# Kernel optimization log

Measured on AMD Instinct MI355X. Metric: run time of the kernel, lower is better.

## Reference

```python
import jax, jax.numpy as jnp
import numpy as np

B, D0, D1 = 4096, 128, 128
T, DEPTH, W = 64, 2, 4          # num_tree, depth, width
S = W ** (DEPTH + 1)            # num_state = 64
NODES = sum(W ** l for l in range(DEPTH + 1))  # 21 internal nodes per tree
D = D0 + D1


def setup_inputs() -> dict:
    key = jax.random.key(0)
    ks = jax.random.split(key, 9)
    inp0 = jax.random.normal(ks[0], (B, D0), jnp.float32)
    inp1 = jax.random.normal(ks[1], (B, D1), jnp.float32)
    x2 = jax.random.normal(ks[2], (B,), jnp.float32)
    # ForestLinear: per-tree, per-node linear maps to `width` branch logits
    W_nodes = 0.02 * jax.random.normal(ks[3], (T, NODES, D, W), jnp.float32)
    b_nodes = jnp.zeros((T, NODES, W), jnp.float32)
    # MultiDense([0,1], 1): per-(tree,state) linear probe per input
    W0 = 0.02 * jax.random.normal(ks[4], (T, S, D0), jnp.float32)
    b0 = jnp.zeros((T, S), jnp.float32)
    W1 = 0.02 * jax.random.normal(ks[5], (T, S, D1), jnp.float32)
    b1 = jnp.zeros((T, S), jnp.float32)
    return {"inp0": inp0, "inp1": inp1, "x2": x2,
            "W_nodes": W_nodes, "b_nodes": b_nodes,
            "W0": W0, "b0": b0, "W1": W1, "b1": b1}


def _forest_states(x, W_nodes, b_nodes):
    # x: [B, D] -> leaf-state probabilities [B, T, S]
    logits = jnp.einsum('bd,tndw->btnw', x, W_nodes) + b_nodes  # [B,T,NODES,W]
    probs = jax.nn.softmax(logits, axis=-1)
    p = jnp.ones((x.shape[0], T, 1), probs.dtype)
    off = 0
    for l in range(DEPTH + 1):
        n = W ** l
        pl = probs[:, :, off:off + n, :]                 # [B,T,n,W]
        p = (p[..., None] * pl).reshape(x.shape[0], T, n * W)
        off += n
    return p  # [B, T, S]


def reference(inp0, inp1, x2, W_nodes, b_nodes, W0, b0, W1, b1):
    x_states = _forest_states(jnp.concatenate([inp0, inp1], axis=-1), W_nodes, b_nodes)
    # per-tree/state linear probes; equivalent to tile + MultiDense, no materialized tile
    x_pred = (jnp.einsum('bd,tsd->bts', inp0, W0) + b0
              + jnp.einsum('bd,tsd->bts', inp1, W1) + b1)  # [B,T,S]
    y_pred_logit_parallel = x2[:, None, None] + x_pred
    ave_pred_tree = jnp.sum(x_states * jax.nn.sigmoid(y_pred_logit_parallel), axis=2)  # [B,T]
    ave_pred = jnp.mean(ave_pred_tree, axis=1)  # [B]
    return (y_pred_logit_parallel, ave_pred)
```

## Files before the change

### kernel.cpp

```cpp
#include <hip/hip_runtime.h>

#define B_SZ    4096
#define DD      256
#define T_TREES 64
#define NNODES  21
#define S_LEAF  64
#define M_TILE  256
#define HBYTES  40960
#define WBYTES  (2 * HBYTES)
#define XOFF    ((size_t)T_TREES * WBYTES)
#define QBYTES  20480


typedef __attribute__((ext_vector_type(8))) short  short8;
typedef __attribute__((ext_vector_type(4))) float  f32x4;

#define DPP_ADD(x, ctrl) ((x) + __int_as_float(__builtin_amdgcn_mov_dpp(__float_as_int(x), (ctrl), 0xF, 0xF, true)))
#define DPP_MOV(x, ctrl) __int_as_float(__builtin_amdgcn_mov_dpp(__float_as_int(x), (ctrl), 0xF, 0xF, true))
__device__ __forceinline__ float qsum4(float x) {
    x = DPP_ADD(x, 0xB1);
    x = DPP_ADD(x, 0x4E);
    return x;
}
__device__ __forceinline__ float rsum16(float x) {
    x = DPP_ADD(x, 0xB1);
    x = DPP_ADD(x, 0x4E);
    x = DPP_ADD(x, 0x124);
    x = DPP_ADD(x, 0x128);
    return x;
}

__device__ __forceinline__ unsigned short f2bf(float f) {
    unsigned int u = __float_as_uint(f);
    u += 0x7fffu + ((u >> 16) & 1u);
    return (unsigned short)(u >> 16);
}
__device__ __forceinline__ void gl2lds16(const void* g, void* l) {
    __builtin_amdgcn_global_load_lds(
        (const __attribute__((address_space(1))) unsigned int*)g,
        (__attribute__((address_space(3))) unsigned int*)l, 16, 0, 0);
}
__device__ __host__ __forceinline__ int woffh(int c, int klo) {
    return c * 256 + (((klo ^ c) & 15) << 4);
}
__device__ __host__ __forceinline__ int woffq(int c, int klo) {
    return (c >> 1) * 256 + (((((klo << 1) ^ (c & 14))) | (c & 1)) << 4);
}

__global__ void zero_ave_kernel(float* __restrict__ out1) {
    int i = blockIdx.x * 256 + threadIdx.x;
    if (i < B_SZ) out1[i] = 0.0f;
}

__global__ void prep_weights(const float* __restrict__ Wn, const float* __restrict__ W0,
                             const float* __restrict__ W1, const float* __restrict__ inp0,
                             const float* __restrict__ inp1, char* __restrict__ ws,
                             float* __restrict__ out1) {
    int id = blockIdx.x * 256 + threadIdx.x;
    if (id < 43008) {
        int oct  = id & 31;
        int rest = id >> 5;
        int n    = rest % NNODES;
        int t    = rest / NNODES;
        int h    = oct >> 4, klo = oct & 15;
        const f32x4* src = (const f32x4*)(Wn + (((size_t)t * NNODES + n) * DD + oct * 8) * 4);
        f32x4 v[8];
        #pragma unroll
        for (int j = 0; j < 8; ++j) v[j] = src[j];
        char* base = ws + (size_t)t * WBYTES + h * HBYTES;
        #pragma unroll
        for (int w = 0; w < 4; ++w) {
            int c = n * 4 + w + (n >= 5 ? 12 : 0);
            short8 pack;
            #pragma unroll
            for (int j = 0; j < 8; ++j) pack[j] = (short)f2bf(v[j][w]);
            *(short8*)(base + woffh(c, klo)) = pack;
        }
    } else if (id < 67584) {
        int idx  = id - 43008;
        int kc   = idx & 31;
        int rest = idx >> 5;
        int c    = 20 + rest % 12;
        int t    = rest / 12;
        short8 z = (short8){0,0,0,0,0,0,0,0};
        *(short8*)(ws + (size_t)t * WBYTES + (kc >> 4) * HBYTES + woffh(c, kc & 15)) = z;
    } else if (id < 198656) {
        int idx = id - 67584;
        int kc  = idx & 31;
        int s   = (idx >> 5) & 63;
        int t   = idx >> 11;
        int k0  = kc * 8;
        const float* src = (k0 < 128) ? (W0 + ((size_t)t * S_LEAF + s) * 128 + k0)
                                      : (W1 + ((size_t)t * S_LEAF + s) * 128 + (k0 - 128));
        short8 pack;
        #pragma unroll
        for (int j = 0; j < 8; ++j) pack[j] = (short)f2bf(src[j]);
        *(short8*)(ws + (size_t)t * WBYTES + (kc >> 4) * HBYTES + woffh(96 + s, kc & 15)) = pack;
    } else if (id < 202752) {
        out1[id - 198656] = 0.0f;
    } else if (id < 333824) {
        int idx = id - 202752;
        int oct = idx & 31;
        int r   = idx >> 5;
        const float* src = (oct < 16) ? (inp0 + (size_t)r * 128 + oct * 8)
                                      : (inp1 + (size_t)r * 128 + (oct - 16) * 8);
        f32x4 f0 = *(const f32x4*)src;
        f32x4 f1 = *(const f32x4*)(src + 4);
        short8 pack;
        pack[0]=(short)f2bf(f0[0]); pack[1]=(short)f2bf(f0[1]);
        pack[2]=(short)f2bf(f0[2]); pack[3]=(short)f2bf(f0[3]);
        pack[4]=(short)f2bf(f1[0]); pack[5]=(short)f2bf(f1[1]);
        pack[6]=(short)f2bf(f1[2]); pack[7]=(short)f2bf(f1[3]);
        *(short8*)(ws + XOFF + ((size_t)r * DD + oct * 8) * 2) = pack;
    }
}

__global__ __launch_bounds__(512, 4)
void forest_main(const float* __restrict__ x2,  const float* __restrict__ bn,
                 const float* __restrict__ b0,  const float* __restrict__ b1,
                 const char* __restrict__ wsW,
                 float* __restrict__ out0, float* __restrict__ out1) {
    __shared__ __align__(16) char smem[HBYTES];

    const int tid  = threadIdx.x;
    const int orig = blockIdx.x;
    const int swz  = (orig & 7) * 128 + (orig >> 3);
    const int t    = swz >> 4;
    const int mt   = swz & 15;
    const int m0   = mt * M_TILE;
    const int lane = tid & 63;
    const int wid  = tid >> 6;
    const int ri   = lane & 15;
    const int kg   = lane >> 4;

    const unsigned short* xbf = (const unsigned short*)(wsW + XOFF);
    const char* wbase = wsW + (size_t)t * WBYTES;

    f32x4 acc[2][10];
    #pragma unroll
    for (int sr = 0; sr < 2; ++sr)
        #pragma unroll
        for (int ct = 0; ct < 10; ++ct)
            acc[sr][ct] = (f32x4){0.f, 0.f, 0.f, 0.f};

    const int gr0r = m0 + wid * 32 + ri;
    const int gr1r = gr0r + 16;
    const unsigned short* aBase0 = xbf + (size_t)gr0r * DD + kg * 8;
    const unsigned short* aBase1 = xbf + (size_t)gr1r * DD + kg * 8;

    for (int h = 0; h < 2; ++h) {
        {
            const char* src = wbase + h * HBYTES + tid * 16;
            char* dst = smem + tid * 16;
            #pragma unroll
            for (int it = 0; it < 5; ++it)
                gl2lds16(src + it * 8192, dst + it * 8192);
        }
        short8 a0 = *(const short8*)(aBase0 + (h * 4) * 32);
        short8 a1 = *(const short8*)(aBase1 + (h * 4) * 32);
        __syncthreads();

        #pragma unroll
        for (int ks = 0; ks < 4; ++ks) {
            short8 n0, n1;
            if (ks < 3) {
                n0 = *(const short8*)(aBase0 + (h * 4 + ks + 1) * 32);
                n1 = *(const short8*)(aBase1 + (h * 4 + ks + 1) * 32);
            }
            const int klo = ks * 4 + kg;
            const int dsB = ri * 256 + (((klo ^ ri) & 15) << 4);
            #pragma unroll
            for (int ct = 0; ct < 10; ++ct) {
                short8 bv = *(const short8*)(smem + dsB + ct * 4096);
                acc[0][ct] = __builtin_amdgcn_mfma_f32_16x16x32_bf16(a0, bv, acc[0][ct], 0, 0, 0);
                acc[1][ct] = __builtin_amdgcn_mfma_f32_16x16x32_bf16(a1, bv, acc[1][ct], 0, 0, 0);
            }
            a0 = n0; a1 = n1;
        }
        if (h == 0) __syncthreads();
    }

    const int kgbase = kg * 16;
    #pragma unroll
    for (int sr = 0; sr < 2; ++sr) {
        const int rlBase = wid * 32 + sr * 16 + kg * 4;
        const int gr0 = m0 + rlBase;
        f32x4 x2v = *(const f32x4*)(x2 + gr0);
        float bn0 = bn[t * 84 + ri];
        float bn1 = bn[t * 84 + 16 + (ri & 3)];

        float L1r[4];
        #pragma unroll
        for (int r = 0; r < 4; ++r) {
            float e0 = __expf(acc[sr][0][r] + bn0);
            float p0 = e0 * __builtin_amdgcn_rcpf(qsum4(e0));
            float e1 = __expf(acc[sr][1][r] + bn1);
            float p1 = e1 * __builtin_amdgcn_rcpf(qsum4(e1));
            float pa  = __shfl(p0, kgbase + (ri >> 2));
            float pb0 = DPP_MOV(p0, 0x124);
            float pb1 = DPP_MOV(p1, 0x124);
            L1r[r] = pa * ((ri < 12) ? pb0 : pb1);
        }
        float partial[4] = {0.f, 0.f, 0.f, 0.f};
        #pragma unroll
        for (int ct = 0; ct < 4; ++ct) {
            int s = ct * 16 + ri;
            float bn2 = bn[t * 84 + 20 + s];
            float bb  = b0[t * S_LEAF + s] + b1[t * S_LEAF + s];
            #pragma unroll
            for (int r = 0; r < 4; ++r) {
                float e = __expf(acc[sr][2 + ct][r] + bn2);
                float p2 = e * __builtin_amdgcn_rcpf(qsum4(e));
                float L2 = p2 * __shfl(L1r[r], kgbase + ct * 4 + (ri >> 2));
                float y = acc[sr][6 + ct][r] + x2v[r] + bb;
                out0[((size_t)(gr0 + r) * T_TREES + t) * S_LEAF + s] = y;
                float sg = __builtin_amdgcn_rcpf(1.0f + __expf(-y));
                partial[r] += sg * L2;
            }
        }
        #pragma unroll
        for (int r = 0; r < 4; ++r) {
            float p = rsum16(partial[r]);
            if (ri == 0) atomicAdd(out1 + gr0 + r, p * (1.0f / T_TREES));
        }
    }
}

__device__ __forceinline__ short8 ldAraw(const float* __restrict__ inp0,
                                         const float* __restrict__ inp1,
                                         int gr, int kkidx, int kg) {
    int k0 = kkidx * 32 + kg * 8;
    const float* src = (k0 < 128) ? (inp0 + (size_t)gr * 128 + k0)
                                  : (inp1 + (size_t)gr * 128 + (k0 - 128));
    f32x4 f0 = *(const f32x4*)src;
    f32x4 f1 = *(const f32x4*)(src + 4);
    short8 a;
    a[0]=(short)f2bf(f0[0]); a[1]=(short)f2bf(f0[1]);
    a[2]=(short)f2bf(f0[2]); a[3]=(short)f2bf(f0[3]);
    a[4]=(short)f2bf(f1[0]); a[5]=(short)f2bf(f1[1]);
    a[6]=(short)f2bf(f1[2]); a[7]=(short)f2bf(f1[3]);
    return a;
}

__global__ __launch_bounds__(256, 2)
void forest_fb(const float* __restrict__ inp0, const float* __restrict__ inp1,
               const float* __restrict__ x2,   const float* __restrict__ Wn,
               const float* __restrict__ bn,   const float* __restrict__ W0,
               const float* __restrict__ b0,   const float* __restrict__ W1,
               const float* __restrict__ b1,
               float* __restrict__ out0, float* __restrict__ out1) {
    __shared__ __align__(16) char smem[QBYTES];

    const int tid  = threadIdx.x;
    const int orig = blockIdx.x;
    const int swz  = (orig & 7) * 256 + (orig >> 3);
    const int t    = swz >> 5;
    const int mt   = swz & 31;
    const int m0   = mt * 128;
    const int lane = tid & 63;
    const int wid  = tid >> 6;
    const int ri   = lane & 15;
    const int kg   = lane >> 4;

    f32x4 acc[2][10];
    #pragma unroll
    for (int sr = 0; sr < 2; ++sr)
        #pragma unroll
        for (int ct = 0; ct < 10; ++ct)
            acc[sr][ct] = (f32x4){0.f, 0.f, 0.f, 0.f};

    const int gr0r = m0 + wid * 32 + ri;
    const int gr1r = gr0r + 16;

    int dsb[2];
    #pragma unroll
    for (int kkl = 0; kkl < 2; ++kkl) {
        int klo = kkl * 4 + kg;
        dsb[kkl] = (ri >> 1) * 256 + (((((klo << 1) ^ (ri & 14))) | (ri & 1)) << 4);
    }

    for (int q = 0; q < 4; ++q) {
        #pragma unroll
        for (int it = 0; it < 5; ++it) {
            int idx = tid + it * 256;
            int c   = idx >> 3;
            int klo = idx & 7;
            int k0  = (q * 8 + klo) * 8;
            unsigned short v[8];
            if (c < 20) {
                int n = c >> 2, w = c & 3;
                const float* src = Wn + (((size_t)t * NNODES + n) * DD + k0) * 4 + w;
                #pragma unroll
                for (int j = 0; j < 8; ++j) v[j] = f2bf(src[j * 4]);
            } else if (c < 32) {
                #pragma unroll
                for (int j = 0; j < 8; ++j) v[j] = 0;
            } else if (c < 96) {
                int n = 5 + ((c - 32) >> 2), w = (c - 32) & 3;
                const float* src = Wn + (((size_t)t * NNODES + n) * DD + k0) * 4 + w;
                #pragma unroll
                for (int j = 0; j < 8; ++j) v[j] = f2bf(src[j * 4]);
            } else {
                int s = c - 96;
                const float* src = (k0 < 128) ? (W0 + ((size_t)t * S_LEAF + s) * 128 + k0)
                                              : (W1 + ((size_t)t * S_LEAF + s) * 128 + (k0 - 128));
                #pragma unroll
                for (int j = 0; j < 8; ++j) v[j] = f2bf(src[j]);
            }
            short8 pack;
            #pragma unroll
            for (int j = 0; j < 8; ++j) pack[j] = (short)v[j];
            *(short8*)(smem + woffq(c, klo)) = pack;
        }
        short8 a00 = ldAraw(inp0, inp1, gr0r, 2*q+0, kg);
        short8 a10 = ldAraw(inp0, inp1, gr1r, 2*q+0, kg);
        short8 a01 = ldAraw(inp0, inp1, gr0r, 2*q+1, kg);
        short8 a11 = ldAraw(inp0, inp1, gr1r, 2*q+1, kg);
        __syncthreads();
        #pragma unroll
        for (int ct = 0; ct < 10; ++ct) {
            short8 b0f = *(const short8*)(smem + dsb[0] + ct * 2048);
            acc[0][ct] = __builtin_amdgcn_mfma_f32_16x16x32_bf16(a00, b0f, acc[0][ct], 0, 0, 0);
            acc[1][ct] = __builtin_amdgcn_mfma_f32_16x16x32_bf16(a10, b0f, acc[1][ct], 0, 0, 0);
        }
        #pragma unroll
        for (int ct = 0; ct < 10; ++ct) {
            short8 b1f = *(const short8*)(smem + dsb[1] + ct * 2048);
            acc[0][ct] = __builtin_amdgcn_mfma_f32_16x16x32_bf16(a01, b1f, acc[0][ct], 0, 0, 0);
            acc[1][ct] = __builtin_amdgcn_mfma_f32_16x16x32_bf16(a11, b1f, acc[1][ct], 0, 0, 0);
        }
        if (q < 3) __syncthreads();
    }

    const int kgbase = kg * 16;
    #pragma unroll
    for (int sr = 0; sr < 2; ++sr) {
        const int rlBase = wid * 32 + sr * 16 + kg * 4;
        const int gr0 = m0 + rlBase;
        f32x4 x2v = *(const f32x4*)(x2 + gr0);
        float bn0 = bn[t * 84 + ri];
        float bn1 = bn[t * 84 + 16 + (ri & 3)];
        float L1r[4];
        #pragma unroll
        for (int r = 0; r < 4; ++r) {
            float e0 = __expf(acc[sr][0][r] + bn0);
            float p0 = e0 * __builtin_amdgcn_rcpf(qsum4(e0));
            float e1 = __expf(acc[sr][1][r] + bn1);
            float p1 = e1 * __builtin_amdgcn_rcpf(qsum4(e1));
            float pa  = __shfl(p0, kgbase + (ri >> 2));
            float pb0 = DPP_MOV(p0, 0x124);
            float pb1 = DPP_MOV(p1, 0x124);
            L1r[r] = pa * ((ri < 12) ? pb0 : pb1);
        }
        float partial[4] = {0.f, 0.f, 0.f, 0.f};
        #pragma unroll
        for (int ct = 0; ct < 4; ++ct) {
            int s = ct * 16 + ri;
            float bn2 = bn[t * 84 + 20 + s];
            float bb  = b0[t * S_LEAF + s] + b1[t * S_LEAF + s];
            #pragma unroll
            for (int r = 0; r < 4; ++r) {
                float e = __expf(acc[sr][2 + ct][r] + bn2);
                float p2 = e * __builtin_amdgcn_rcpf(qsum4(e));
                float L2 = p2 * __shfl(L1r[r], kgbase + ct * 4 + (ri >> 2));
                float y = acc[sr][6 + ct][r] + x2v[r] + bb;
                out0[((size_t)(gr0 + r) * T_TREES + t) * S_LEAF + s] = y;
                float sg = __builtin_amdgcn_rcpf(1.0f + __expf(-y));
                partial[r] += sg * L2;
            }
        }
        #pragma unroll
        for (int r = 0; r < 4; ++r) {
            float p = rsum16(partial[r]);
            if (ri == 0) atomicAdd(out1 + gr0 + r, p * (1.0f / T_TREES));
        }
    }
}

extern "C" void kernel_launch(void* const* d_in, const int* in_sizes, int n_in,
                              void* d_out, int out_size, void* d_ws, size_t ws_size,
                              hipStream_t stream) {
    const float* inp0 = (const float*)d_in[0];
    const float* inp1 = (const float*)d_in[1];
    const float* x2   = (const float*)d_in[2];
    const float* Wn   = (const float*)d_in[3];
    const float* bn   = (const float*)d_in[4];
    const float* W0   = (const float*)d_in[5];
    const float* b0   = (const float*)d_in[6];
    const float* W1   = (const float*)d_in[7];
    const float* b1   = (const float*)d_in[8];

    float* out0 = (float*)d_out;
    float* out1 = out0 + (size_t)B_SZ * T_TREES * S_LEAF;

    const size_t need = XOFF + (size_t)B_SZ * DD * 2;

    if (ws_size >= need) {
        hipLaunchKernelGGL(prep_weights, dim3(1304), dim3(256), 0, stream,
                           Wn, W0, W1, inp0, inp1, (char*)d_ws, out1);
        hipLaunchKernelGGL(forest_main, dim3((B_SZ / M_TILE) * T_TREES), dim3(512), 0, stream,
                           x2, bn, b0, b1, (const char*)d_ws, out0, out1);
    } else {
        hipLaunchKernelGGL(zero_ave_kernel, dim3((B_SZ + 255) / 256), dim3(256), 0, stream, out1);
        hipLaunchKernelGGL(forest_fb, dim3((B_SZ / 128) * T_TREES), dim3(256), 0, stream,
                           inp0, inp1, x2, Wn, bn, W0, b0, W1, b1, out0, out1);
    }
}
```

Baseline: 53.43 us.

## Switch main GEMM to 32x32x16 MFMA tiles and restructure epilogue

Replaces the 16x16x32 bf16 MFMA tiling (two row sub-tiles by ten column tiles per wave) with 32x32x16 MFMA tiles (five 32-column tiles per wave, 16 accumulators each). This halves the number of LDS B-fragment loads per K step and removes the second A-operand load stream. The epilogue is rewritten for the new accumulator layout: root and level-1 softmax probabilities come from one tile, path products are built by shuffles, and the final reduction combines the two half-rows with DPP before the atomic add. Launch bounds drop from 4 to 3 waves-per-EU minimum, which allows more registers per thread but can lower occupancy.

```diff
diff --git a/kernel.cpp b/kernel.cpp
--- a/kernel.cpp
+++ b/kernel.cpp
@@ -12,8 +12,9 @@
 #define QBYTES  20480
 
 
-typedef __attribute__((ext_vector_type(8))) short  short8;
-typedef __attribute__((ext_vector_type(4))) float  f32x4;
+typedef __attribute__((ext_vector_type(8)))  short short8;
+typedef __attribute__((ext_vector_type(4)))  float f32x4;
+typedef __attribute__((ext_vector_type(16))) float f32x16;
 
 #define DPP_ADD(x, ctrl) ((x) + __int_as_float(__builtin_amdgcn_mov_dpp(__float_as_int(x), (ctrl), 0xF, 0xF, true)))
 #define DPP_MOV(x, ctrl) __int_as_float(__builtin_amdgcn_mov_dpp(__float_as_int(x), (ctrl), 0xF, 0xF, true))
@@ -115,7 +116,7 @@
     }
 }
 
-__global__ __launch_bounds__(512, 4)
+__global__ __launch_bounds__(512, 3)
 void forest_main(const float* __restrict__ x2,  const float* __restrict__ bn,
                  const float* __restrict__ b0,  const float* __restrict__ b1,
                  const char* __restrict__ wsW,
@@ -130,23 +131,21 @@
     const int m0   = mt * M_TILE;
     const int lane = tid & 63;
     const int wid  = tid >> 6;
-    const int ri   = lane & 15;
-    const int kg   = lane >> 4;
+    const int cl   = lane & 31;
+    const int hi   = lane >> 5;
 
     const unsigned short* xbf = (const unsigned short*)(wsW + XOFF);
     const char* wbase = wsW + (size_t)t * WBYTES;
 
-    f32x4 acc[2][10];
-    #pragma unroll
-    for (int sr = 0; sr < 2; ++sr)
-        #pragma unroll
-        for (int ct = 0; ct < 10; ++ct)
-            acc[sr][ct] = (f32x4){0.f, 0.f, 0.f, 0.f};
-
-    const int gr0r = m0 + wid * 32 + ri;
-    const int gr1r = gr0r + 16;
-    const unsigned short* aBase0 = xbf + (size_t)gr0r * DD + kg * 8;
-    const unsigned short* aBase1 = xbf + (size_t)gr1r * DD + kg * 8;
+    f32x16 acc[5];
+    #pragma unroll
+    for (int ct = 0; ct < 5; ++ct)
+        #pragma unroll
+        for (int j = 0; j < 16; ++j)
+            acc[ct][j] = 0.0f;
+
+    const int arow = m0 + wid * 32 + cl;
+    const unsigned short* aBase = xbf + (size_t)arow * DD + hi * 8;
 
     for (int h = 0; h < 2; ++h) {
         {
@@ -156,73 +155,60 @@
             for (int it = 0; it < 5; ++it)
                 gl2lds16(src + it * 8192, dst + it * 8192);
         }
-        short8 a0 = *(const short8*)(aBase0 + (h * 4) * 32);
-        short8 a1 = *(const short8*)(aBase1 + (h * 4) * 32);
+        short8 a = *(const short8*)(aBase + h * 128);
         __syncthreads();
 
         #pragma unroll
-        for (int ks = 0; ks < 4; ++ks) {
-            short8 n0, n1;
-            if (ks < 3) {
-                n0 = *(const short8*)(aBase0 + (h * 4 + ks + 1) * 32);
-                n1 = *(const short8*)(aBase1 + (h * 4 + ks + 1) * 32);
+        for (int kk = 0; kk < 8; ++kk) {
+            short8 an;
+            if (kk < 7)
+                an = *(const short8*)(aBase + h * 128 + (kk + 1) * 16);
+            const int chunk = kk * 2 + hi;
+            #pragma unroll
+            for (int ct = 0; ct < 5; ++ct) {
+                const int c = ct * 32 + cl;
+                short8 bv = *(const short8*)(smem + c * 256 + (((chunk ^ c) & 15) << 4));
+                acc[ct] = __builtin_amdgcn_mfma_f32_32x32x16_bf16(a, bv, acc[ct], 0, 0, 0);
             }
-            const int klo = ks * 4 + kg;
-            const int dsB = ri * 256 + (((klo ^ ri) & 15) << 4);
-            #pragma unroll
-            for (int ct = 0; ct < 10; ++ct) {
-                short8 bv = *(const short8*)(smem + dsB + ct * 4096);
-                acc[0][ct] = __builtin_amdgcn_mfma_f32_16x16x32_bf16(a0, bv, acc[0][ct], 0, 0, 0);
-                acc[1][ct] = __builtin_amdgcn_mfma_f32_16x16x32_bf16(a1, bv, acc[1][ct], 0, 0, 0);
-            }
-            a0 = n0; a1 = n1;
+            a = an;
         }
         if (h == 0) __syncthreads();
     }
 
-    const int kgbase = kg * 16;
-    #pragma unroll
-    for (int sr = 0; sr < 2; ++sr) {
-        const int rlBase = wid * 32 + sr * 16 + kg * 4;
-        const int gr0 = m0 + rlBase;
-        f32x4 x2v = *(const f32x4*)(x2 + gr0);
-        float bn0 = bn[t * 84 + ri];
-        float bn1 = bn[t * 84 + 16 + (ri & 3)];
-
-        float L1r[4];
-        #pragma unroll
-        for (int r = 0; r < 4; ++r) {
-            float e0 = __expf(acc[sr][0][r] + bn0);
-            float p0 = e0 * __builtin_amdgcn_rcpf(qsum4(e0));
-            float e1 = __expf(acc[sr][1][r] + bn1);
-            float p1 = e1 * __builtin_amdgcn_rcpf(qsum4(e1));
-            float pa  = __shfl(p0, kgbase + (ri >> 2));
-            float pb0 = DPP_MOV(p0, 0x124);
-            float pb1 = DPP_MOV(p1, 0x124);
-            L1r[r] = pa * ((ri < 12) ? pb0 : pb1);
-        }
-        float partial[4] = {0.f, 0.f, 0.f, 0.f};
-        #pragma unroll
-        for (int ct = 0; ct < 4; ++ct) {
-            int s = ct * 16 + ri;
-            float bn2 = bn[t * 84 + 20 + s];
-            float bb  = b0[t * S_LEAF + s] + b1[t * S_LEAF + s];
-            #pragma unroll
-            for (int r = 0; r < 4; ++r) {
-                float e = __expf(acc[sr][2 + ct][r] + bn2);
-                float p2 = e * __builtin_amdgcn_rcpf(qsum4(e));
-                float L2 = p2 * __shfl(L1r[r], kgbase + ct * 4 + (ri >> 2));
-                float y = acc[sr][6 + ct][r] + x2v[r] + bb;
-                out0[((size_t)(gr0 + r) * T_TREES + t) * S_LEAF + s] = y;
-                float sg = __builtin_amdgcn_rcpf(1.0f + __expf(-y));
-                partial[r] += sg * L2;
-            }
-        }
-        #pragma unroll
-        for (int r = 0; r < 4; ++r) {
-            float p = rsum16(partial[r]);
-            if (ri == 0) atomicAdd(out1 + gr0 + r, p * (1.0f / T_TREES));
-        }
+    const int hbase = hi << 5;
+    float bnv  = (cl < 20) ? bn[t * 84 + cl] : 0.0f;
+    float bn2a = bn[t * 84 + 20 + cl];
+    float bn2b = bn[t * 84 + 52 + cl];
+    float bba  = b0[t * S_LEAF + cl]      + b1[t * S_LEAF + cl];
+    float bbb  = b0[t * S_LEAF + 32 + cl] + b1[t * S_LEAF + 32 + cl];
+    const int gpa0 = hbase + (cl >> 4);
+    const int gpb0 = hbase + 4 + (cl >> 2);
+    const int gpa1 = hbase + 2 + (cl >> 4);
+    const int gpb1 = hbase + 12 + (cl >> 2);
+    const int rbase = m0 + wid * 32 + 4 * hi;
+
+    #pragma unroll
+    for (int reg = 0; reg < 16; ++reg) {
+        const int grow = rbase + (reg & 3) + 8 * (reg >> 2);
+        float e0 = __expf(acc[0][reg] + bnv);
+        float p0 = e0 * __builtin_amdgcn_rcpf(qsum4(e0));
+        float eL0 = __expf(acc[1][reg] + bn2a);
+        float pL0 = eL0 * __builtin_amdgcn_rcpf(qsum4(eL0));
+        float eL1 = __expf(acc[2][reg] + bn2b);
+        float pL1 = eL1 * __builtin_amdgcn_rcpf(qsum4(eL1));
+        float L20 = pL0 * __shfl(p0, gpa0) * __shfl(p0, gpb0);
+        float L21 = pL1 * __shfl(p0, gpa1) * __shfl(p0, gpb1);
+        float xv = x2[grow];
+        float y0 = acc[3][reg] + xv + bba;
+        float y1 = acc[4][reg] + xv + bbb;
+        out0[((size_t)grow * T_TREES + t) * S_LEAF + cl]      = y0;
+        out0[((size_t)grow * T_TREES + t) * S_LEAF + 32 + cl] = y1;
+        float sg0 = __builtin_amdgcn_rcpf(1.0f + __expf(-y0));
+        float sg1 = __builtin_amdgcn_rcpf(1.0f + __expf(-y1));
+        float contrib = sg0 * L20 + sg1 * L21;
+        float s = rsum16(contrib);
+        float bsum = s + DPP_MOV(s, 0x142);
+        if (cl == 16) atomicAdd(out1 + grow, bsum * (1.0f / T_TREES));
     }
 }
 
```

New measurement: 53.46 us. About the same (+0.1%).
